# Optimization experiments

Measured on AMD Instinct MI355X. Metric: run time of the kernel, lower is better.

Reference implementation:

```python
import jax, jax.numpy as jnp
import numpy as np

B, C, H, W = 8, 256, 64, 64   # batch, num_hiddens, spatial
N, D = 1024, 256              # n_embed, embedding_dim
TEMP = 1.0                    # temp_init


def setup_inputs() -> dict:
    key = jax.random.key(0)
    k1, k2, k3 = jax.random.split(key, 3)
    z = jax.random.normal(k1, (B, C, H, W), dtype=jnp.float32)
    # 1x1 conv == per-pixel linear: weight [n_embed, num_hiddens], bias [n_embed]
    proj_w = jax.random.normal(k2, (N, C), dtype=jnp.float32) * 0.02
    proj_b = jnp.zeros((N,), dtype=jnp.float32)
    embed = jax.random.normal(k3, (N, D), dtype=jnp.float32) * 0.02
    return {"z": z, "proj_w": proj_w, "proj_b": proj_b, "embed": embed}


def reference(z, proj_w, proj_b, embed):
    # logits = Conv2d(num_hiddens, n_embed, 1)(z)  -> [b, n, h, w]
    logits = jnp.einsum('bchw,nc->bnhw', z, proj_w) + proj_b[None, :, None, None]
    # argmax_softmax (straight-through) over the codebook axis (dim=1), tau=TEMP
    y_soft = jax.nn.softmax(logits / TEMP, axis=1)
    ind = jnp.argmax(y_soft, axis=1)  # [b, h, w]
    y_hard = jax.nn.one_hot(ind, N, axis=1, dtype=logits.dtype)  # [b, n, h, w]
    soft_one_hot = y_hard - jax.lax.stop_gradient(y_soft) + y_soft
    # z_q = einsum('b n h w, n d -> b d h w', soft_one_hot, embed)
    z_q = jnp.einsum('bnhw,nd->bdhw', soft_one_hot, embed)
    diff = jnp.zeros((1,), dtype=logits.dtype)
    return (z_q, diff, ind)
```

## Files before the change

### kernel.cpp

```cpp
#include <hip/hip_runtime.h>
#include <math.h>

#define HWP 4096
#define CCH 256
#define NN  1024
#define DD  256
#define ZQ_SIZE (8 * DD * HWP)
#define MARGIN 2e-3f
#define WLCAP 4096

typedef _Float16 h8 __attribute__((ext_vector_type(8)));
typedef float    f4 __attribute__((ext_vector_type(4)));

__global__ __launch_bounds__(256) void split_w_k(
    const float* __restrict__ w, _Float16* __restrict__ whS,
    int* __restrict__ wcount)
{
    if (blockIdx.x == 0 && threadIdx.x == 0) *wcount = 0;
    const int t = blockIdx.x * 256 + threadIdx.x;
    const int l = t & 63;
    const int frag = t >> 6;
    const int kc = frag & 7, r16 = frag >> 3;
    const int row = r16 * 16 + (l & 15);
    const int c   = kc * 32 + (l >> 4) * 8;
    const float* src = w + (size_t)row * CCH + c;
    _Float16 hv[8];
#pragma unroll
    for (int j = 0; j < 8; ++j) hv[j] = (_Float16)src[j];
    *(h8*)(whS + (size_t)t * 8) = *(const h8*)hv;
}

__global__ __launch_bounds__(512, 4) void mfma_gemm_k(
    const float* __restrict__ z,
    const _Float16* __restrict__ whS,
    const float* __restrict__ bias, const float* __restrict__ embed,
    int* __restrict__ wcount, int* __restrict__ wlist,
    float* __restrict__ out)
{
    __shared__ __align__(16) char smem[71680];
    __shared__ int indsh2[64];
    float* s_best = (float*)(smem + 65536);
    float* s_sec  = (float*)(smem + 67584);
    int*   s_idx  = (int*)  (smem + 69632);

    const int tid = threadIdx.x;
    const int l   = tid & 63;
    const int wv  = tid >> 6;
    const int mh  = wv >> 2;
    const int ng  = wv & 3;
    const int c15 = l & 15, g = l >> 4;
    const int pix0 = blockIdx.x * 64;
    const int b = pix0 >> 12, p0 = pix0 & 4095;

    {
        const int px = tid & 63;
        const int wv2 = tid >> 6;
        const int p16 = px >> 4;
        const float* zb = z + (size_t)b * CCH * HWP + p0 + px;
#pragma unroll
        for (int it = 0; it < 4; ++it) {
            const int cg = wv2 * 4 + it;
            const int c = cg * 8;
            float xv[8];
#pragma unroll
            for (int i = 0; i < 8; ++i) xv[i] = zb[(size_t)(c + i) * HWP];
            _Float16 hv[8], lv[8];
#pragma unroll
            for (int i = 0; i < 8; ++i) {
                const _Float16 h = (_Float16)xv[i];
                hv[i] = h;
                lv[i] = (_Float16)(xv[i] - (float)h);
            }
            const int kc = cg >> 2;
            const int lane = (px & 15) + 16 * (cg & 3);
            const int off = ((p16 * 8 + kc) * 64 + lane) * 16;
            *(h8*)(smem + off)         = *(const h8*)hv;
            *(h8*)(smem + 32768 + off) = *(const h8*)lv;
        }
    }
    __syncthreads();

    float best[8], sec[8]; int bidx[8];
#pragma unroll
    for (int s = 0; s < 8; ++s) { best[s] = -INFINITY; sec[s] = -INFINITY; bidx[s] = 0; }

#pragma unroll 1
    for (int nt = 0; nt < 4; ++nt) {
        const int n0 = nt * 256 + ng * 64;
        const int r16_0 = n0 >> 4;
        f4 acc[2][4];
#pragma unroll
        for (int mf = 0; mf < 2; ++mf)
#pragma unroll
            for (int nf = 0; nf < 4; ++nf) acc[mf][nf] = (f4)0.f;

#pragma unroll 2
        for (int kc = 0; kc < 8; ++kc) {
            h8 ah[2], al[2], bh[4];
#pragma unroll
            for (int mf = 0; mf < 2; ++mf) {
                const int ao = (((mh * 2 + mf) * 8 + kc) * 64 + l) * 16;
                ah[mf] = *(const h8*)(smem + ao);
                al[mf] = *(const h8*)(smem + 32768 + ao);
            }
#pragma unroll
            for (int nf = 0; nf < 4; ++nf) {
                const size_t bo = (((size_t)(r16_0 + nf) * 8 + kc) * 64 + l) * 8;
                bh[nf] = *(const h8*)(whS + bo);
            }
#pragma unroll
            for (int mf = 0; mf < 2; ++mf)
#pragma unroll
                for (int nf = 0; nf < 4; ++nf) {
                    acc[mf][nf] = __builtin_amdgcn_mfma_f32_16x16x32_f16(ah[mf], bh[nf], acc[mf][nf], 0, 0, 0);
                    acc[mf][nf] = __builtin_amdgcn_mfma_f32_16x16x32_f16(al[mf], bh[nf], acc[mf][nf], 0, 0, 0);
                }
        }
#pragma unroll
        for (int nf = 0; nf < 4; ++nf) {
            const int n_abs = n0 + nf * 16 + c15;
            const float bv = bias[n_abs];
#pragma unroll
            for (int mf = 0; mf < 2; ++mf)
#pragma unroll
                for (int r = 0; r < 4; ++r) {
                    const float v = acc[mf][nf][r] + bv;
                    const int s = mf * 4 + r;
                    if (v > best[s]) { sec[s] = best[s]; best[s] = v; bidx[s] = n_abs; }
                    else if (v > sec[s]) sec[s] = v;
                }
        }
    }

#pragma unroll
    for (int d = 1; d < 16; d <<= 1) {
#pragma unroll
        for (int s = 0; s < 8; ++s) {
            const float ob = __shfl_xor(best[s], d, 64);
            const float os = __shfl_xor(sec[s], d, 64);
            const int   oi = __shfl_xor(bidx[s], d, 64);
            if (ob > best[s])       { sec[s] = fmaxf(best[s], os); best[s] = ob; bidx[s] = oi; }
            else if (ob == best[s]) { sec[s] = ob; bidx[s] = (oi < bidx[s]) ? oi : bidx[s]; }
            else                    { sec[s] = fmaxf(sec[s], ob); }
        }
    }
#pragma unroll
    for (int s = 0; s < 8; ++s) {
        if (c15 == s) {
            const int px = (mh * 2 + (s >> 2)) * 16 + g * 4 + (s & 3);
            s_best[wv * 64 + px] = best[s];
            s_sec [wv * 64 + px] = sec[s];
            s_idx [wv * 64 + px] = bidx[s];
        }
    }
    __syncthreads();
    if (tid < 64) {
        const int wb = (tid >> 5) * 4;
        float b0 = s_best[wb * 64 + tid], s0 = s_sec[wb * 64 + tid]; int i0 = s_idx[wb * 64 + tid];
#pragma unroll
        for (int c = 1; c < 4; ++c) {
            const float ob = s_best[(wb + c) * 64 + tid], os = s_sec[(wb + c) * 64 + tid];
            const int   oi = s_idx [(wb + c) * 64 + tid];
            if (ob > b0 || (ob == b0 && oi < i0)) { s0 = fmaxf(b0, os); b0 = ob; i0 = oi; }
            else                                  { s0 = fmaxf(s0, ob); }
        }
        const int pix = pix0 + tid;
        indsh2[tid] = i0;
        out[ZQ_SIZE + 1 + pix] = (float)i0;
        if (b0 - s0 < MARGIN) {
            const int pos = atomicAdd(wcount, 1);
            if (pos < WLCAP) wlist[pos] = pix;
        }
    }
    if (blockIdx.x == 0 && tid == 0) out[ZQ_SIZE] = 0.0f;
    __syncthreads();

    float (*tile)[257] = (float (*)[257])smem;
    const int lq = tid & 63, wq = tid >> 6;
    const int l32 = tid & 31, dq = tid >> 5;
#pragma unroll 1
    for (int pp = 0; pp < 2; ++pp) {
#pragma unroll
        for (int it = 0; it < 4; ++it) {
            const int pl = it * 8 + wq;
            const int row = indsh2[pp * 32 + pl];
            const float4 e = *(const float4*)(embed + (size_t)row * DD + lq * 4);
            tile[pl][lq * 4 + 0] = e.x;
            tile[pl][lq * 4 + 1] = e.y;
            tile[pl][lq * 4 + 2] = e.z;
            tile[pl][lq * 4 + 3] = e.w;
        }
        __syncthreads();
        float* outz = out + (size_t)b * DD * HWP + p0 + pp * 32;
#pragma unroll
        for (int dd = 0; dd < 16; ++dd) {
            const int d = dd * 16 + dq;
            outz[(size_t)d * HWP + l32] = tile[l32][d];
        }
        __syncthreads();
    }
}

__global__ __launch_bounds__(256) void fixup_k(
    const float* __restrict__ z, const float* __restrict__ w,
    const float* __restrict__ bias, const float* __restrict__ embed,
    const int* __restrict__ wcount, const int* __restrict__ wlist,
    float* __restrict__ out)
{
    __shared__ float zsh[4][256];
    __shared__ float m_v[4][4];
    __shared__ int   m_i[4][4];
    __shared__ int   s_i[4];

    const int tid = threadIdx.x;
    const int l = tid & 63, wv = tid >> 6;
    const int c15 = l & 15, q = l >> 4;
    int nw = *wcount;
    if (nw > WLCAP) nw = WLCAP;
    if (nw < 0) nw = 0;
    const int ntask = (nw + 3) >> 2;

    for (int t = blockIdx.x; t < ntask; t += 512) {
        const int e0 = t * 4;
        const int npx = (nw - e0 < 4) ? (nw - e0) : 4;
        int pixv[4];
#pragma unroll
        for (int px = 0; px < 4; ++px) {
            const int e = e0 + ((px < npx) ? px : (npx - 1));
            pixv[px] = wlist[e];
        }
        __syncthreads();
#pragma unroll
        for (int px = 0; px < 4; ++px) {
            const int pix = pixv[px];
            const int b = pix >> 12, p = pix & 4095;
            zsh[px][tid] = z[((size_t)b * CCH + tid) * HWP + p];
        }
        __syncthreads();

        float best[4]; int bi[4];
#pragma unroll
        for (int px = 0; px < 4; ++px) { best[px] = -INFINITY; bi[px] = 0; }

        for (int g16 = 0; g16 < 16; ++g16) {
            const int row = wv * 256 + g16 * 16 + c15;
            const float* wr = w + (size_t)row * CCH + q * 64;
            float part[4] = {0.f, 0.f, 0.f, 0.f};
#pragma unroll
            for (int j = 0; j < 16; ++j) {
                const float4 w4 = *(const float4*)(wr + j * 4);
#pragma unroll
                for (int px = 0; px < 4; ++px) {
                    const float4 z4 = *(const float4*)&zsh[px][q * 64 + j * 4];
                    part[px] = fmaf(w4.x, z4.x, part[px]);
                    part[px] = fmaf(w4.y, z4.y, part[px]);
                    part[px] = fmaf(w4.z, z4.z, part[px]);
                    part[px] = fmaf(w4.w, z4.w, part[px]);
                }
            }
            const float bv = bias[row];
#pragma unroll
            for (int px = 0; px < 4; ++px) {
                float pv = part[px];
                pv += __shfl_xor(pv, 16, 64);
                pv += __shfl_xor(pv, 32, 64);
                const float v = pv + bv;
                if (v > best[px]) { best[px] = v; bi[px] = row; }
            }
        }
#pragma unroll
        for (int d = 1; d < 16; d <<= 1) {
#pragma unroll
            for (int px = 0; px < 4; ++px) {
                const float ob = __shfl_xor(best[px], d, 64);
                const int   oi = __shfl_xor(bi[px], d, 64);
                if (ob > best[px] || (ob == best[px] && oi < bi[px])) { best[px] = ob; bi[px] = oi; }
            }
        }
        if (l == 0) {
#pragma unroll
            for (int px = 0; px < 4; ++px) { m_v[wv][px] = best[px]; m_i[wv][px] = bi[px]; }
        }
        __syncthreads();
        if (tid < 4) {
            float v = m_v[0][tid]; int i = m_i[0][tid];
#pragma unroll
            for (int t2 = 1; t2 < 4; ++t2)
                if (m_v[t2][tid] > v || (m_v[t2][tid] == v && m_i[t2][tid] < i)) { v = m_v[t2][tid]; i = m_i[t2][tid]; }
            s_i[tid] = i;
            if (tid < npx) out[ZQ_SIZE + 1 + pixv[tid]] = (float)i;
        }
        __syncthreads();
        for (int px = 0; px < npx; ++px) {
            const int pix = pixv[px];
            const int b = pix >> 12, p = pix & 4095;
            out[((size_t)b * DD + tid) * HWP + p] = embed[(size_t)s_i[px] * DD + tid];
        }
    }
}

extern "C" void kernel_launch(void* const* d_in, const int* in_sizes, int n_in,
                              void* d_out, int out_size, void* d_ws, size_t ws_size,
                              hipStream_t stream) {
    const float* z     = (const float*)d_in[0];
    const float* w     = (const float*)d_in[1];
    const float* bias  = (const float*)d_in[2];
    const float* embed = (const float*)d_in[3];
    float* out = (float*)d_out;

    _Float16* whS = (_Float16*)d_ws;
    int* wcount = (int*)((char*)d_ws + 524288);
    int* wlist  = (int*)((char*)d_ws + 524544);

    hipLaunchKernelGGL(split_w_k,   dim3(128), dim3(256), 0, stream, w, whS, wcount);
    hipLaunchKernelGGL(mfma_gemm_k, dim3(512), dim3(512), 0, stream,
                       z, whS, bias, embed, wcount, wlist, out);
    hipLaunchKernelGGL(fixup_k,     dim3(512), dim3(256), 0, stream,
                       z, w, bias, embed, wcount, wlist, out);
}
```

Measured before the change: 190.7 us.

## Split fixup argmax across codebook chunks with atomic 64-bit max merge

The fixup kernel now gives each block 8 pixels and one of 8 chunks of 128 codebook rows, instead of 4 pixels over all 1024 rows, and launches 1024 blocks. Partial argmaxes are merged with a packed 64-bit atomicMax keyed on an order-preserving float encoding, with ties going to the lower index. The last block per pixel group, detected by an atomic counter, writes the index and the gathered embedding. The aim is more parallelism and a shorter serial loop when the list of near-tie pixels is small, at the cost of atomics, extra workspace clearing and a threadfence.

```diff
diff --git a/kernel.cpp b/kernel.cpp
--- a/kernel.cpp
+++ b/kernel.cpp
@@ -8,16 +8,21 @@
 #define ZQ_SIZE (8 * DD * HWP)
 #define MARGIN 2e-3f
 #define WLCAP 4096
+#define NCH 8
+#define PXB 8
 
 typedef _Float16 h8 __attribute__((ext_vector_type(8)));
 typedef float    f4 __attribute__((ext_vector_type(4)));
 
 __global__ __launch_bounds__(256) void split_w_k(
     const float* __restrict__ w, _Float16* __restrict__ whS,
-    int* __restrict__ wcount)
+    int* __restrict__ wcount, unsigned long long* __restrict__ fin,
+    int* __restrict__ pgdone)
 {
-    if (blockIdx.x == 0 && threadIdx.x == 0) *wcount = 0;
     const int t = blockIdx.x * 256 + threadIdx.x;
+    if (t == 0) *wcount = 0;
+    if (t < WLCAP) fin[t] = 0ULL;
+    if (t < 512)  pgdone[t] = 0;
     const int l = t & 63;
     const int frag = t >> 6;
     const int kc = frag & 7, r16 = frag >> 3;
@@ -205,12 +210,14 @@
     const float* __restrict__ z, const float* __restrict__ w,
     const float* __restrict__ bias, const float* __restrict__ embed,
     const int* __restrict__ wcount, const int* __restrict__ wlist,
+    unsigned long long* __restrict__ fin, int* __restrict__ pgdone,
     float* __restrict__ out)
 {
-    __shared__ float zsh[4][256];
-    __shared__ float m_v[4][4];
-    __shared__ int   m_i[4][4];
-    __shared__ int   s_i[4];
+    __shared__ float zsh[PXB][256];
+    __shared__ float m_v[4][PXB];
+    __shared__ int   m_i[4][PXB];
+    __shared__ int   s_idx[PXB];
+    __shared__ int   s_fin;
 
     const int tid = threadIdx.x;
     const int l = tid & 63, wv = tid >> 6;
@@ -218,39 +225,43 @@
     int nw = *wcount;
     if (nw > WLCAP) nw = WLCAP;
     if (nw < 0) nw = 0;
-    const int ntask = (nw + 3) >> 2;
-
-    for (int t = blockIdx.x; t < ntask; t += 512) {
-        const int e0 = t * 4;
-        const int npx = (nw - e0 < 4) ? (nw - e0) : 4;
-        int pixv[4];
-#pragma unroll
-        for (int px = 0; px < 4; ++px) {
-            const int e = e0 + ((px < npx) ? px : (npx - 1));
-            pixv[px] = wlist[e];
-        }
-        __syncthreads();
-#pragma unroll
-        for (int px = 0; px < 4; ++px) {
+    const int npg = (nw + PXB - 1) / PXB;
+    const int ntask = npg * NCH;
+
+    for (int t = blockIdx.x; t < ntask; t += 1024) {
+        const int pg = t >> 3, ck = t & 7;
+        const int e0 = pg * PXB;
+        const int npx = (nw - e0 < PXB) ? (nw - e0) : PXB;
+        int pixv[PXB];
+#pragma unroll
+        for (int px = 0; px < PXB; ++px)
+            pixv[px] = wlist[e0 + ((px < npx) ? px : (npx - 1))];
+
+        __syncthreads();
+#pragma unroll
+        for (int px = 0; px < PXB; ++px) {
             const int pix = pixv[px];
             const int b = pix >> 12, p = pix & 4095;
             zsh[px][tid] = z[((size_t)b * CCH + tid) * HWP + p];
         }
         __syncthreads();
 
-        float best[4]; int bi[4];
-#pragma unroll
-        for (int px = 0; px < 4; ++px) { best[px] = -INFINITY; bi[px] = 0; }
-
-        for (int g16 = 0; g16 < 16; ++g16) {
-            const int row = wv * 256 + g16 * 16 + c15;
+        float best[PXB]; int bi[PXB];
+#pragma unroll
+        for (int px = 0; px < PXB; ++px) { best[px] = -INFINITY; bi[px] = 0; }
+
+#pragma unroll
+        for (int g16 = 0; g16 < 2; ++g16) {
+            const int row = ck * 128 + wv * 32 + g16 * 16 + c15;
             const float* wr = w + (size_t)row * CCH + q * 64;
-            float part[4] = {0.f, 0.f, 0.f, 0.f};
+            float part[PXB];
+#pragma unroll
+            for (int px = 0; px < PXB; ++px) part[px] = 0.f;
 #pragma unroll
             for (int j = 0; j < 16; ++j) {
                 const float4 w4 = *(const float4*)(wr + j * 4);
 #pragma unroll
-                for (int px = 0; px < 4; ++px) {
+                for (int px = 0; px < PXB; ++px) {
                     const float4 z4 = *(const float4*)&zsh[px][q * 64 + j * 4];
                     part[px] = fmaf(w4.x, z4.x, part[px]);
                     part[px] = fmaf(w4.y, z4.y, part[px]);
@@ -260,7 +271,7 @@
             }
             const float bv = bias[row];
 #pragma unroll
-            for (int px = 0; px < 4; ++px) {
+            for (int px = 0; px < PXB; ++px) {
                 float pv = part[px];
                 pv += __shfl_xor(pv, 16, 64);
                 pv += __shfl_xor(pv, 32, 64);
@@ -271,7 +282,7 @@
 #pragma unroll
         for (int d = 1; d < 16; d <<= 1) {
 #pragma unroll
-            for (int px = 0; px < 4; ++px) {
+            for (int px = 0; px < PXB; ++px) {
                 const float ob = __shfl_xor(best[px], d, 64);
                 const int   oi = __shfl_xor(bi[px], d, 64);
                 if (ob > best[px] || (ob == best[px] && oi < bi[px])) { best[px] = ob; bi[px] = oi; }
@@ -279,22 +290,40 @@
         }
         if (l == 0) {
 #pragma unroll
-            for (int px = 0; px < 4; ++px) { m_v[wv][px] = best[px]; m_i[wv][px] = bi[px]; }
-        }
-        __syncthreads();
-        if (tid < 4) {
+            for (int px = 0; px < PXB; ++px) { m_v[wv][px] = best[px]; m_i[wv][px] = bi[px]; }
+        }
+        __syncthreads();
+        if (tid < npx) {
             float v = m_v[0][tid]; int i = m_i[0][tid];
 #pragma unroll
             for (int t2 = 1; t2 < 4; ++t2)
                 if (m_v[t2][tid] > v || (m_v[t2][tid] == v && m_i[t2][tid] < i)) { v = m_v[t2][tid]; i = m_i[t2][tid]; }
-            s_i[tid] = i;
-            if (tid < npx) out[ZQ_SIZE + 1 + pixv[tid]] = (float)i;
-        }
-        __syncthreads();
-        for (int px = 0; px < npx; ++px) {
-            const int pix = pixv[px];
-            const int b = pix >> 12, p = pix & 4095;
-            out[((size_t)b * DD + tid) * HWP + p] = embed[(size_t)s_i[px] * DD + tid];
+            const unsigned int s = __float_as_uint(v);
+            const unsigned int key = (s & 0x80000000u) ? ~s : (s | 0x80000000u);
+            const unsigned long long enc =
+                ((unsigned long long)key << 32) | (unsigned long long)(~(unsigned int)i);
+            atomicMax(&fin[e0 + tid], enc);
+        }
+        __syncthreads();
+        if (tid == 0) {
+            __threadfence();
+            const int old = atomicAdd(&pgdone[pg], 1);
+            s_fin = (old == NCH - 1) ? 1 : 0;
+        }
+        __syncthreads();
+        if (s_fin) {
+            if (tid < npx) {
+                const unsigned long long cur = atomicMax(&fin[e0 + tid], 0ULL);
+                const int idx = (int)(~(unsigned int)cur);
+                s_idx[tid] = idx;
+                out[ZQ_SIZE + 1 + pixv[tid]] = (float)idx;
+            }
+            __syncthreads();
+            for (int px = 0; px < npx; ++px) {
+                const int pix = pixv[px];
+                const int b = pix >> 12, p = pix & 4095;
+                out[((size_t)b * DD + tid) * HWP + p] = embed[(size_t)s_idx[px] * DD + tid];
+            }
         }
     }
 }
@@ -311,10 +340,12 @@
     _Float16* whS = (_Float16*)d_ws;
     int* wcount = (int*)((char*)d_ws + 524288);
     int* wlist  = (int*)((char*)d_ws + 524544);
-
-    hipLaunchKernelGGL(split_w_k,   dim3(128), dim3(256), 0, stream, w, whS, wcount);
+    unsigned long long* fin = (unsigned long long*)((char*)d_ws + 540928);
+    int* pgdone = (int*)((char*)d_ws + 573696);
+
+    hipLaunchKernelGGL(split_w_k,   dim3(128), dim3(256), 0, stream, w, whS, wcount, fin, pgdone);
     hipLaunchKernelGGL(mfma_gemm_k, dim3(512), dim3(512), 0, stream,
                        z, whS, bias, embed, wcount, wlist, out);
-    hipLaunchKernelGGL(fixup_k,     dim3(512), dim3(256), 0, stream,
-                       z, w, bias, embed, wcount, wlist, out);
+    hipLaunchKernelGGL(fixup_k,     dim3(1024), dim3(256), 0, stream,
+                       z, w, bias, embed, wcount, wlist, fin, pgdone, out);
 }
```

Result: slower. 200.9 us (+5.3%).
